# Optimization experiments

Measured on AMD Instinct MI355X. Metric: run time of the kernel, lower is better.

Reference implementation:

```python
import jax, jax.numpy as jnp
import numpy as np

B, N, D_IN, H, D_H, D_OUT = 2, 1024, 1024, 16, 64, 1024
NEG = -1e9


def skew_relative(QE_t):
    # QE_t: [B, H, N, 2N-1] -> [B, H, N, N] via the pad/reshape skew trick
    b, h, n = QE_t.shape[0], QE_t.shape[1], QE_t.shape[2]
    x = jnp.pad(QE_t, ((0, 0), (0, 0), (0, 0), (0, 1)))          # [B,H,N,2N]
    x = x.reshape(b, h, -1)                                       # [B,H,2N^2]
    x = jnp.pad(x, ((0, 0), (0, 0), (0, n - 1)))                  # [B,H,(N+1)(2N-1)]
    x = x.reshape(b, h, n + 1, 2 * n - 1)
    return x[:, :, :n, -n:]


def setup_inputs() -> dict:
    key = jax.random.key(0)
    ks = jax.random.split(key, 8)
    x = jax.random.normal(ks[0], (B, N, D_IN), dtype=jnp.float32)
    E_rel = jax.random.normal(ks[1], (2 * N - 1, D_H), dtype=jnp.float32)
    # additive causal mask [1,1,N,N]
    causal = jnp.tril(jnp.ones((N, N), dtype=bool))
    mask = jnp.where(causal, 0.0, NEG).astype(jnp.float32)[None, None]
    s = 1.0 / np.sqrt(D_IN)
    Wq = jax.random.normal(ks[2], (D_IN, H * D_H), dtype=jnp.float32) * s
    Wk = jax.random.normal(ks[3], (D_IN, H * D_H), dtype=jnp.float32) * s
    Wv = jax.random.normal(ks[4], (D_IN, H * D_H), dtype=jnp.float32) * s
    Wo = jax.random.normal(ks[5], (H * D_H, D_OUT), dtype=jnp.float32) * (1.0 / np.sqrt(H * D_H))
    bo = jnp.zeros((D_OUT,), dtype=jnp.float32)
    return {"x": x, "E_rel": E_rel, "mask": mask, "Wq": Wq, "Wk": Wk, "Wv": Wv, "Wo": Wo, "bo": bo}


def reference(x, E_rel, mask, Wq, Wk, Wv, Wo, bo):
    b = x.shape[0]
    scale = 1.0 / np.sqrt(D_H)
    # project and split heads -> [B, H, N, d]
    Q = (x @ Wq).reshape(b, -1, H, D_H).transpose(0, 2, 1, 3)
    K = (x @ Wk).reshape(b, -1, H, D_H).transpose(0, 2, 1, 3)
    V = (x @ Wv).reshape(b, -1, H, D_H).transpose(0, 2, 1, 3)
    attn = jnp.einsum('bhnd,bhmd->bhnm', Q, K)                    # [B,H,N,N]
    QE_t = jnp.einsum('bhnd,rd->bhnr', Q, E_rel)                  # [B,H,N,2N-1]
    attn = (attn + skew_relative(QE_t)) * scale + mask
    attn = jax.nn.softmax(attn, axis=-1)
    out = jnp.einsum('bhnm,bhmd->bhnd', attn, V)                  # [B,H,N,d]
    out = out.transpose(0, 2, 1, 3).reshape(b, -1, H * D_H)
    return out @ Wo + bo  # dropout is identity at inference
```

## Files before the change

### kernel.cpp

```cpp
#include <hip/hip_runtime.h>
#include <cstdint>
#include <cstddef>

typedef __bf16 bf16;
typedef __bf16 bf16x8 __attribute__((ext_vector_type(8)));
typedef float  f32x4  __attribute__((ext_vector_type(4)));

#define MFMA16(a,b,c) __builtin_amdgcn_mfma_f32_16x16x32_bf16((a),(b),(c),0,0,0)

__device__ __forceinline__ void gload_lds16(const bf16* g, bf16* l) {
  __builtin_amdgcn_global_load_lds((__attribute__((address_space(1))) void*)(g),
                                   (__attribute__((address_space(3))) void*)(l),
                                   16, 0, 0);
}

__global__ __launch_bounds__(256) void prep_k(
    const float* __restrict__ x, const float* __restrict__ E,
    const float* __restrict__ W0, const float* __restrict__ W1,
    const float* __restrict__ W2, const float* __restrict__ W3,
    bf16* __restrict__ xb, bf16* __restrict__ Eb, bf16* __restrict__ Wt) {
  __shared__ float t[32][33];
  const int bid = blockIdx.x;
  const int tid = threadIdx.x;
  if (bid < 2176) {
    const bool isx = (bid < 2048);
    const float* src = isx ? x : E;
    bf16* dst = isx ? xb : Eb;
    const int n = isx ? (2048 * 1024) : (2047 * 64);
    const int i = (isx ? bid : (bid - 2048)) * 1024 + tid * 4;
    if (i < n) {
      float4 v = *(const float4*)(src + i);
      dst[i + 0] = (bf16)v.x;
      dst[i + 1] = (bf16)v.y;
      dst[i + 2] = (bf16)v.z;
      dst[i + 3] = (bf16)v.w;
    }
  } else {
    const int tt = bid - 2176;
    const int z = tt >> 10;
    const int rem = tt & 1023;
    const int cx = (rem & 31) * 32;
    const int ry = (rem >> 5) * 32;
    const float* src = (z == 0) ? W0 : (z == 1) ? W1 : (z == 2) ? W2 : W3;
    bf16* dst = Wt + (size_t)z * (1024 * 1024);
    const int xx = tid & 31, yy = tid >> 5;
    #pragma unroll
    for (int j = 0; j < 32; j += 8) t[yy + j][xx] = src[(size_t)(ry + yy + j) * 1024 + cx + xx];
    __syncthreads();
    #pragma unroll
    for (int j = 0; j < 32; j += 8)
      dst[(size_t)(cx + yy + j) * 1024 + ry + xx] = (bf16)t[xx][yy + j];
  }
}

template <int RM, int RN>
__global__ __launch_bounds__(512, 4) void gemm512(
    const bf16* __restrict__ A, const bf16* __restrict__ Bt,
    bf16* __restrict__ QKV, float* __restrict__ Of,
    const float* __restrict__ bias, const int mode) {
  constexpr int K = 1024;
  constexpr int MT = 2 * RM * 16;
  constexpr int NT = 4 * RN * 16;
  const int row0 = blockIdx.x * MT;
  const int col0 = blockIdx.y * NT;

  __shared__ bf16 As[2][MT * 64];
  __shared__ bf16 Bs[2][NT * 64];

  const int tid = threadIdx.x;
  const int lane = tid & 63;
  const int wid = tid >> 6;
  const int wr = wid >> 2, wc = wid & 3;
  const int lr = lane & 15;
  const int g  = lane >> 4;
  const int srow8 = lane >> 3;
  const int scol = ((lane & 7) ^ srow8) * 8;

  f32x4 acc[RM][RN];
  #pragma unroll
  for (int a = 0; a < RM; ++a)
    #pragma unroll
    for (int b = 0; b < RN; ++b) acc[a][b] = (f32x4){0.f, 0.f, 0.f, 0.f};

  auto stg = [&](int bb, int k0_) {
    constexpr int ARW = MT / 8;
    #pragma unroll
    for (int q = 0; q < ARW / 8; ++q)
      gload_lds16(A + (size_t)(row0 + wid * ARW + q * 8 + srow8) * K + k0_ + scol,
                  &As[bb][(wid * ARW + q * 8) * 64]);
    #pragma unroll
    for (int q = 0; q < 2; ++q)
      gload_lds16(Bt + (size_t)(col0 + wid * 16 + q * 8 + srow8) * K + k0_ + scol,
                  &Bs[bb][(wid * 16 + q * 8) * 64]);
  };

  stg(0, 0);
  for (int t = 0; t < K / 64; ++t) {
    __syncthreads();
    if (t + 1 < K / 64) stg((t + 1) & 1, (t + 1) * 64);
    const bf16* as = &As[t & 1][0];
    const bf16* bs = &Bs[t & 1][0];
    bf16x8 af[RM][2], bfv[RN][2];
    #pragma unroll
    for (int mi = 0; mi < RM; ++mi)
      #pragma unroll
      for (int kk = 0; kk < 2; ++kk)
        af[mi][kk] = *(const bf16x8*)&as[(wr * RM * 16 + mi * 16 + lr) * 64 +
                                         ((kk * 32 + g * 8) ^ ((lr & 7) << 3))];
    #pragma unroll
    for (int ni = 0; ni < RN; ++ni)
      #pragma unroll
      for (int kk = 0; kk < 2; ++kk)
        bfv[ni][kk] = *(const bf16x8*)&bs[(wc * RN * 16 + ni * 16 + lr) * 64 +
                                          ((kk * 32 + g * 8) ^ ((lr & 7) << 3))];
    #pragma unroll
    for (int mi = 0; mi < RM; ++mi)
      #pragma unroll
      for (int ni = 0; ni < RN; ++ni)
        #pragma unroll
        for (int kk = 0; kk < 2; ++kk)
          acc[mi][ni] = MFMA16(af[mi][kk], bfv[ni][kk], acc[mi][ni]);
  }

  #pragma unroll
  for (int mi = 0; mi < RM; ++mi) {
    #pragma unroll
    for (int ni = 0; ni < RN; ++ni) {
      #pragma unroll
      for (int r = 0; r < 4; ++r) {
        const int row = row0 + wr * RM * 16 + mi * 16 + g * 4 + r;
        const int col = col0 + wc * RN * 16 + ni * 16 + lr;
        const float v = acc[mi][ni][r];
        if (mode == 2) {
          Of[(size_t)row * 1024 + col] = v + bias[col];
        } else {
          const int b = row >> 10, i = row & 1023;
          const int which = col >> 10, cc = col & 1023;
          const int h = cc >> 6, d = cc & 63;
          if (which < 2)
            QKV[(size_t)which * 2097152 + (((size_t)(b * 16 + h)) * 1024 + i) * 64 + d] = (bf16)v;
          else
            QKV[(size_t)2 * 2097152 + (((size_t)(b * 16 + h)) * 64 + d) * 1024 + i] = (bf16)v;
        }
      }
    }
  }
}

__device__ const int CH_QB[36] = {7,7,7,7,7,7,7, 6,6,6,6,6,6, 5,5,5,5,5, 4,4,4,4,
                                  3,3,3, 2,2, 1, 0,1,2,3,4,5,6,7};
__device__ const int CH_K0[36] = {0,2,4,6,8,10,12, 0,2,4,6,8,10, 0,2,4,6,8, 0,2,4,6,
                                  0,2,4, 0,2, 0, 0,2,4,6,8,10,12,14};
__device__ const int QB_P0[8] = {0,1,3,6,10,15,21,28};

__global__ __launch_bounds__(512, 4) void attn_kernel(
    const bf16* __restrict__ Qh, const bf16* __restrict__ Kh,
    const bf16* __restrict__ Vt, const bf16* __restrict__ Eb,
    bf16* __restrict__ OP, float* __restrict__ LP) {
  constexpr int N = 1024;
  const int flat = blockIdx.y * 36 + blockIdx.x;
  const int task = (flat & 7) * 144 + (flat >> 3);
  const int bh = task / 36;
  const int ch = task - bh * 36;
  const int qb = CH_QB[ch];
  const int kb0 = CH_K0[ch];
  const int i0 = qb * 128;

  const bf16* Qp = Qh + (size_t)bh * N * 64;
  const bf16* Kp = Kh + (size_t)bh * N * 64;
  const bf16* Vp = Vt + (size_t)bh * 64 * N;

  __shared__ bf16 Ks[2][64 * 64];
  __shared__ bf16 Vs[2][64 * 64];
  __shared__ bf16 Es[256 * 64];
  __shared__ bf16 Psm[8][16 * 64];

  const int tid = threadIdx.x;
  const int lane = tid & 63;
  const int wid = tid >> 6;
  const int lr = lane & 15;
  const int g  = lane >> 4;
  const int iw0 = i0 + wid * 16;
  bf16* pp = &Psm[wid][0];

  const int srow8 = lane >> 3;
  const int sch = ((lane & 7) ^ srow8) * 8;

  bf16x8 qf[2];
  {
    const bf16* qrow = Qp + (size_t)(iw0 + lr) * 64 + g * 8;
    qf[0] = *(const bf16x8*)(qrow);
    qf[1] = *(const bf16x8*)(qrow + 32);
  }

  float lb[4] = {0.f, 0.f, 0.f, 0.f};
  f32x4 oacc[4];
  #pragma unroll
  for (int r = 0; r < 4; ++r) oacc[r] = (f32x4){0.f, 0.f, 0.f, 0.f};

  constexpr float SC = 0.18033688f;
  const int fb = 7 - wid;
  const int j0a = kb0 * 64;
  const int ebase0 = (N - 128) + j0a - i0;

  auto STAGE_KV = [&](int b, int j0) {
    gload_lds16(Kp + (size_t)(j0 + wid * 8 + srow8) * 64 + sch, &Ks[b][(wid * 8) * 64]);
    gload_lds16(Vp + (size_t)(wid * 8 + srow8) * 1024 + j0 + sch, &Vs[b][(wid * 8) * 64]);
  };
  auto STAGE_E = [&]() {
    #pragma unroll
    for (int q = 0; q < 4; ++q)
      gload_lds16(Eb + (size_t)(ebase0 + wid * 32 + q * 8 + srow8) * 64 + sch,
                  &Es[(wid * 32 + q * 8) * 64]);
  };

  auto TILE = [&](int buf, int j0, int eoff) {
    if (j0 > iw0 + 15) return;
    const bf16* kbuf = &Ks[buf][0];
    const bf16* vbuf = &Vs[buf][0];
    f32x4 sa[4];
    #pragma unroll
    for (int ni = 0; ni < 4; ++ni) sa[ni] = (f32x4){0.f, 0.f, 0.f, 0.f};
    __builtin_amdgcn_s_setprio(1);
    #pragma unroll
    for (int ni = 0; ni < 4; ++ni)
      #pragma unroll
      for (int kk = 0; kk < 2; ++kk) {
        bf16x8 kf = *(const bf16x8*)&kbuf[(ni * 16 + lr) * 64 +
                                          ((kk * 32 + g * 8) ^ ((lr & 7) << 3))];
        sa[ni] = MFMA16(qf[kk], kf, sa[ni]);
      }
    f32x4 ea[5];
    #pragma unroll
    for (int s5 = 0; s5 < 5; ++s5) {
      const int er = eoff + (fb + s5) * 16 + lr;
      ea[s5] = (f32x4){0.f, 0.f, 0.f, 0.f};
      bf16x8 e0 = *(const bf16x8*)&Es[er * 64 + ((g * 8) ^ ((lr & 7) << 3))];
      bf16x8 e1 = *(const bf16x8*)&Es[er * 64 + ((32 + g * 8) ^ ((lr & 7) << 3))];
      ea[s5] = MFMA16(qf[0], e0, ea[s5]);
      ea[s5] = MFMA16(qf[1], e1, ea[s5]);
    }
    __builtin_amdgcn_s_setprio(0);
    #pragma unroll
    for (int r = 0; r < 4; ++r) {
      const int di = g * 4 + r;
      const int sl = (g << 4) | ((lr - di - 1) & 15);
      const float sh0 = __shfl(ea[0][r], sl);
      const float sh1 = __shfl(ea[1][r], sl);
      const float sh2 = __shfl(ea[2][r], sl);
      const float sh3 = __shfl(ea[3][r], sl);
      const float sh4 = __shfl(ea[4][r], sl);
      const bool hi = (lr > di);
      const float rel[4] = {hi ? sh1 : sh0, hi ? sh2 : sh1, hi ? sh3 : sh2, hi ? sh4 : sh3};
      const int ig = iw0 + di;
      #pragma unroll
      for (int ni = 0; ni < 4; ++ni) {
        float tv = (sa[ni][r] + rel[ni]) * SC;
        tv = (j0 + ni * 16 + lr > ig) ? -1e30f : tv;
        const float pv = exp2f(tv);
        lb[r] += pv;
        pp[di * 64 + ((ni * 16 + lr) ^ ((di & 7) << 3))] = (bf16)pv;
      }
    }
    bf16x8 pf[2];
    pf[0] = *(const bf16x8*)&pp[lr * 64 + ((g * 8) ^ ((lr & 7) << 3))];
    pf[1] = *(const bf16x8*)&pp[lr * 64 + ((32 + g * 8) ^ ((lr & 7) << 3))];
    __builtin_amdgcn_s_setprio(1);
    #pragma unroll
    for (int nd = 0; nd < 4; ++nd)
      #pragma unroll
      for (int kk = 0; kk < 2; ++kk) {
        bf16x8 vf = *(const bf16x8*)&vbuf[(nd * 16 + lr) * 64 +
                                          ((kk * 32 + g * 8) ^ ((lr & 7) << 3))];
        oacc[nd] = MFMA16(pf[kk], vf, oacc[nd]);
      }
    __builtin_amdgcn_s_setprio(0);
  };

  STAGE_E();
  STAGE_KV(0, j0a);
  STAGE_KV(1, j0a + 64);
  __syncthreads();
  TILE(0, j0a, 0);
  TILE(1, j0a + 64, 64);

  #pragma unroll
  for (int off = 1; off < 16; off <<= 1)
    #pragma unroll
    for (int r = 0; r < 4; ++r)
      lb[r] += __shfl_xor(lb[r], off);

  const int pslot = bh * 36 + QB_P0[qb] + (kb0 >> 1);
  bf16* Op = OP + (size_t)pslot * 8192;
  #pragma unroll
  for (int nd = 0; nd < 4; ++nd)
    #pragma unroll
    for (int r = 0; r < 4; ++r)
      Op[(size_t)(wid * 16 + g * 4 + r) * 64 + nd * 16 + lr] = (bf16)oacc[nd][r];
  if (lr == 0) {
    #pragma unroll
    for (int r = 0; r < 4; ++r)
      LP[pslot * 128 + wid * 16 + g * 4 + r] = lb[r];
  }
}

__global__ __launch_bounds__(256) void merge_k(const bf16* __restrict__ OP,
                                               const float* __restrict__ LP,
                                               bf16* __restrict__ AO) {
  const int bh = blockIdx.x;
  const int qb = blockIdx.y;
  const int half = blockIdx.z;
  const int np = qb + 1;
  const int tid = threadIdx.x;
  const int row = half * 64 + (tid >> 2);
  const int c0 = (tid & 3) * 16;
  const int p0 = bh * 36 + QB_P0[qb];

  float o[16];
  #pragma unroll
  for (int j = 0; j < 16; ++j) o[j] = 0.f;
  float l = 0.f;
  for (int c = 0; c < np; ++c) {
    l += LP[(p0 + c) * 128 + row];
    const bf16* Oc = OP + (size_t)(p0 + c) * 8192 + row * 64 + c0;
    #pragma unroll
    for (int j = 0; j < 16; j += 8) {
      const bf16x8 v = *(const bf16x8*)&Oc[j];
      #pragma unroll
      for (int u = 0; u < 8; ++u) o[j + u] += (float)v[u];
    }
  }
  const float inv = 1.f / l;

  const int b = bh >> 4, h = bh & 15;
  bf16* dst = AO + ((size_t)(b * 1024) + qb * 128 + row) * 1024 + h * 64 + c0;
  #pragma unroll
  for (int j = 0; j < 16; ++j) dst[j] = (bf16)(o[j] * inv);
}

extern "C" void kernel_launch(void* const* d_in, const int* in_sizes, int n_in,
                              void* d_out, int out_size, void* d_ws, size_t ws_size,
                              hipStream_t stream) {
  const float* x  = (const float*)d_in[0];
  const float* E  = (const float*)d_in[1];
  const float* Wq = (const float*)d_in[3];
  const float* Wk = (const float*)d_in[4];
  const float* Wv = (const float*)d_in[5];
  const float* Wo = (const float*)d_in[6];
  const float* bo = (const float*)d_in[7];

  bf16* xb  = (bf16*)d_ws;
  bf16* Wqt = xb + 2048 * 1024;
  bf16* Wot = Wqt + 3 * 1024 * 1024;
  bf16* Eb  = Wqt + 4 * 1024 * 1024;
  bf16* Qh  = Eb + 2048 * 64;
  bf16* AO  = Qh + 3 * 2048 * 1024;
  bf16* OPb = AO + 2048 * 1024;
  float* LPp = (float*)(OPb + (size_t)1152 * 8192);
  float* out = (float*)d_out;

  prep_k<<<dim3(6272), dim3(256), 0, stream>>>(x, E, Wq, Wk, Wv, Wo, xb, Eb, Wqt);

  gemm512<4, 2><<<dim3(16, 24), dim3(512), 0, stream>>>(xb, Wqt, Qh, nullptr, nullptr, 0);

  attn_kernel<<<dim3(36, 32), dim3(512), 0, stream>>>(
      Qh, Qh + 2048 * 1024, Qh + 2 * 2048 * 1024, Eb, OPb, LPp);

  merge_k<<<dim3(32, 8, 2), dim3(256), 0, stream>>>(OPb, LPp, AO);

  gemm512<2, 2><<<dim3(32, 8), dim3(512), 0, stream>>>(AO, Wot, nullptr, out, bo, 2);
}
```

Baseline: 83.22 us.

## Load E fragments from global, pack shuffles to bf16, swizzle GEMM blocks, raise occupancy

```diff
diff --git a/kernel.cpp b/kernel.cpp
--- a/kernel.cpp
+++ b/kernel.cpp
@@ -5,6 +5,7 @@
 typedef __bf16 bf16;
 typedef __bf16 bf16x8 __attribute__((ext_vector_type(8)));
 typedef float  f32x4  __attribute__((ext_vector_type(4)));
+typedef unsigned int u32;
 
 #define MFMA16(a,b,c) __builtin_amdgcn_mfma_f32_16x16x32_bf16((a),(b),(c),0,0,0)
 
@@ -12,6 +13,15 @@
   __builtin_amdgcn_global_load_lds((__attribute__((address_space(1))) void*)(g),
                                    (__attribute__((address_space(3))) void*)(l),
                                    16, 0, 0);
+}
+
+__device__ __forceinline__ u32 pkbf(float a, float b) {
+  union { bf16 h; unsigned short s; } ua, ub;
+  ua.h = (bf16)a; ub.h = (bf16)b;
+  return (u32)ua.s | ((u32)ub.s << 16);
+}
+__device__ __forceinline__ float bf2f(u32 lo16) {
+  union { u32 u; float f; } v; v.u = lo16 << 16; return v.f;
 }
 
 __global__ __launch_bounds__(256) void prep_k(
@@ -61,8 +71,13 @@
   constexpr int K = 1024;
   constexpr int MT = 2 * RM * 16;
   constexpr int NT = 4 * RN * 16;
-  const int row0 = blockIdx.x * MT;
-  const int col0 = blockIdx.y * NT;
+  const int nb = gridDim.x * gridDim.y;
+  int flat = blockIdx.y * gridDim.x + blockIdx.x;
+  flat = (flat & 7) * (nb >> 3) + (flat >> 3);
+  const int bx = flat % gridDim.x;
+  const int by = flat / gridDim.x;
+  const int row0 = bx * MT;
+  const int col0 = by * NT;
 
   __shared__ bf16 As[2][MT * 64];
   __shared__ bf16 Bs[2][NT * 64];
@@ -153,7 +168,7 @@
                                   0,2,4, 0,2, 0, 0,2,4,6,8,10,12,14};
 __device__ const int QB_P0[8] = {0,1,3,6,10,15,21,28};
 
-__global__ __launch_bounds__(512, 4) void attn_kernel(
+__global__ __launch_bounds__(512, 6) void attn_kernel(
     const bf16* __restrict__ Qh, const bf16* __restrict__ Kh,
     const bf16* __restrict__ Vt, const bf16* __restrict__ Eb,
     bf16* __restrict__ OP, float* __restrict__ LP) {
@@ -172,7 +187,6 @@
 
   __shared__ bf16 Ks[2][64 * 64];
   __shared__ bf16 Vs[2][64 * 64];
-  __shared__ bf16 Es[256 * 64];
   __shared__ bf16 Psm[8][16 * 64];
 
   const int tid = threadIdx.x;
@@ -207,17 +221,18 @@
     gload_lds16(Kp + (size_t)(j0 + wid * 8 + srow8) * 64 + sch, &Ks[b][(wid * 8) * 64]);
     gload_lds16(Vp + (size_t)(wid * 8 + srow8) * 1024 + j0 + sch, &Vs[b][(wid * 8) * 64]);
   };
-  auto STAGE_E = [&]() {
-    #pragma unroll
-    for (int q = 0; q < 4; ++q)
-      gload_lds16(Eb + (size_t)(ebase0 + wid * 32 + q * 8 + srow8) * 64 + sch,
-                  &Es[(wid * 32 + q * 8) * 64]);
-  };
 
   auto TILE = [&](int buf, int j0, int eoff) {
     if (j0 > iw0 + 15) return;
     const bf16* kbuf = &Ks[buf][0];
     const bf16* vbuf = &Vs[buf][0];
+    bf16x8 eA[5], eB[5];
+    #pragma unroll
+    for (int s5 = 0; s5 < 5; ++s5) {
+      const bf16* ep = Eb + (size_t)(ebase0 + eoff + (fb + s5) * 16 + lr) * 64 + g * 8;
+      eA[s5] = *(const bf16x8*)(ep);
+      eB[s5] = *(const bf16x8*)(ep + 32);
+    }
     f32x4 sa[4];
     #pragma unroll
     for (int ni = 0; ni < 4; ++ni) sa[ni] = (f32x4){0.f, 0.f, 0.f, 0.f};
@@ -233,25 +248,22 @@
     f32x4 ea[5];
     #pragma unroll
     for (int s5 = 0; s5 < 5; ++s5) {
-      const int er = eoff + (fb + s5) * 16 + lr;
       ea[s5] = (f32x4){0.f, 0.f, 0.f, 0.f};
-      bf16x8 e0 = *(const bf16x8*)&Es[er * 64 + ((g * 8) ^ ((lr & 7) << 3))];
-      bf16x8 e1 = *(const bf16x8*)&Es[er * 64 + ((32 + g * 8) ^ ((lr & 7) << 3))];
-      ea[s5] = MFMA16(qf[0], e0, ea[s5]);
-      ea[s5] = MFMA16(qf[1], e1, ea[s5]);
+      ea[s5] = MFMA16(qf[0], eA[s5], ea[s5]);
+      ea[s5] = MFMA16(qf[1], eB[s5], ea[s5]);
     }
     __builtin_amdgcn_s_setprio(0);
     #pragma unroll
     for (int r = 0; r < 4; ++r) {
       const int di = g * 4 + r;
       const int sl = (g << 4) | ((lr - di - 1) & 15);
-      const float sh0 = __shfl(ea[0][r], sl);
-      const float sh1 = __shfl(ea[1][r], sl);
-      const float sh2 = __shfl(ea[2][r], sl);
-      const float sh3 = __shfl(ea[3][r], sl);
-      const float sh4 = __shfl(ea[4][r], sl);
+      const u32 s01 = (u32)__shfl((int)pkbf(ea[0][r], ea[1][r]), sl);
+      const u32 s23 = (u32)__shfl((int)pkbf(ea[2][r], ea[3][r]), sl);
+      const float s4 = __shfl(ea[4][r], sl);
+      const float e0 = bf2f(s01 & 0xffffu), e1 = bf2f(s01 >> 16);
+      const float e2 = bf2f(s23 & 0xffffu), e3 = bf2f(s23 >> 16);
       const bool hi = (lr > di);
-      const float rel[4] = {hi ? sh1 : sh0, hi ? sh2 : sh1, hi ? sh3 : sh2, hi ? sh4 : sh3};
+      const float rel[4] = {hi ? e1 : e0, hi ? e2 : e1, hi ? e3 : e2, hi ? s4 : e3};
       const int ig = iw0 + di;
       #pragma unroll
       for (int ni = 0; ni < 4; ++ni) {
@@ -277,7 +289,6 @@
     __builtin_amdgcn_s_setprio(0);
   };
 
-  STAGE_E();
   STAGE_KV(0, j0a);
   STAGE_KV(1, j0a + 64);
   __syncthreads();
```

Result: slower. 112.1 us (+34.7%).
